# Kernel tuning notes

Measured on AMD Instinct MI355X. Metric: run time of the kernel, lower is better.

## Reference

```python
import jax, jax.numpy as jnp
import numpy as np

# Dimensions per init_kwargs
B, S, D = 2, 2048, 1024          # batch, seq, hidden_size
F = 4096                          # intermediate_size
E, K = 8, 2                       # moe_num_experts, moe_top_k
EPS = 1e-9


def setup_inputs() -> dict:
    key = jax.random.key(0)
    k1, k2, k3, k4 = jax.random.split(key, 4)
    x = jax.random.normal(k1, (B, S, D), dtype=jnp.float32)
    # gate: Linear(D, E, bias=False) -> stored as [D, E] for x @ w_gate
    w_gate = jax.random.normal(k2, (D, E), dtype=jnp.float32) * 0.02
    # per-expert gate_up_proj: Linear(D, 2F, bias=False), stacked over experts -> [E, D, 2F]
    w_gate_up = jax.random.normal(k3, (E, D, 2 * F), dtype=jnp.float32) * 0.02
    # per-expert down_proj: Linear(F, D, bias=False), stacked -> [E, F, D]
    w_down = jax.random.normal(k4, (E, F, D), dtype=jnp.float32) * 0.02
    return {"x": x, "w_gate": w_gate, "w_gate_up": w_gate_up, "w_down": w_down}


def reference(x, w_gate, w_gate_up, w_down):
    # Router
    gate_logits = x @ w_gate                       # [B,S,E]
    gate_probs = jax.nn.softmax(gate_logits, axis=-1)
    # top-k masking + renormalization (top_k < num_experts)
    topk_vals, topk_idx = jax.lax.top_k(gate_probs, K)           # [B,S,K]
    masked = jnp.sum(jax.nn.one_hot(topk_idx, E, dtype=gate_probs.dtype)
                     * topk_vals[..., None], axis=-2)            # [B,S,E]
    denom = jnp.maximum(jnp.sum(masked, axis=-1, keepdims=True), EPS)
    gate_probs = masked / denom

    # Dense per-expert SwiGLU FFN on all tokens (faithful to reference impl)
    gu = jnp.einsum('bsd,edh->ebsh', x, w_gate_up)               # [E,B,S,2F]
    g, u = jnp.split(gu, 2, axis=-1)                             # [E,B,S,F] each
    act = jax.nn.silu(g) * u                                     # [E,B,S,F]
    expert_out = jnp.einsum('ebsf,efd->ebsd', act, w_down)       # [E,B,S,D]

    # Gate-weighted combine
    return jnp.einsum('bse,ebsd->bsd', gate_probs, expert_out)   # [B,S,D]
```

## Files before the change

### kernel.cpp

```cpp
#include <hip/hip_runtime.h>
#include <stdint.h>

#define NTOK 4096
#define DMODEL 1024
#define FF 4096
#define NEXP 8

typedef __bf16 bf16x8 __attribute__((ext_vector_type(8)));
typedef float f32x4 __attribute__((ext_vector_type(4)));

__device__ __forceinline__ unsigned short f2bf(float f) {
  union { float f; unsigned u; } v; v.f = f;
  unsigned r = v.u + 0x7fffu + ((v.u >> 16) & 1u);
  return (unsigned short)(r >> 16);
}

__global__ __launch_bounds__(256) void k_convert_x(const float4* __restrict__ in,
                                                   ushort4* __restrict__ out, int n4) {
  int stride = gridDim.x * blockDim.x;
  for (int i = blockIdx.x * blockDim.x + threadIdx.x; i < n4; i += stride) {
    float4 v = in[i];
    out[i] = make_ushort4(f2bf(v.x), f2bf(v.y), f2bf(v.z), f2bf(v.w));
  }
}

__global__ __launch_bounds__(256) void k_transpose_bf16(const float* __restrict__ in,
                                                        unsigned short* __restrict__ out,
                                                        int R, int C) {
  __shared__ float tile[64][65];
  const size_t slab = (size_t)R * C;
  const float* ip = in + slab * blockIdx.z;
  unsigned short* op = out + slab * blockIdx.z;
  int c0 = blockIdx.x * 64, r0 = blockIdx.y * 64;
  int tx = threadIdx.x & 15, ty = threadIdx.x >> 4;
#pragma unroll
  for (int i = 0; i < 4; ++i) {
    int r = ty + 16 * i;
    float4 v = *(const float4*)(ip + (size_t)(r0 + r) * C + c0 + tx * 4);
    tile[r][tx * 4 + 0] = v.x;
    tile[r][tx * 4 + 1] = v.y;
    tile[r][tx * 4 + 2] = v.z;
    tile[r][tx * 4 + 3] = v.w;
  }
  __syncthreads();
#pragma unroll
  for (int i = 0; i < 4; ++i) {
    int q = ty + 16 * i;
    ushort4 o = make_ushort4(f2bf(tile[tx * 4 + 0][q]), f2bf(tile[tx * 4 + 1][q]),
                             f2bf(tile[tx * 4 + 2][q]), f2bf(tile[tx * 4 + 3][q]));
    *(ushort4*)(op + (size_t)(c0 + q) * R + r0 + tx * 4) = o;
  }
}

__global__ __launch_bounds__(256) void k_router(const float* __restrict__ x,
                                                const float* __restrict__ wg,
                                                int* __restrict__ cnt,
                                                int* __restrict__ elist,
                                                float* __restrict__ gw) {
  int wave = threadIdx.x >> 6, lane = threadIdx.x & 63;
  int t = blockIdx.x * 4 + wave;
  const float* xp = x + (size_t)t * DMODEL;
  float a[8] = {0, 0, 0, 0, 0, 0, 0, 0};
#pragma unroll
  for (int i = 0; i < DMODEL / 64; ++i) {
    int d = lane + 64 * i;
    float xv = xp[d];
    float4 w0 = *(const float4*)(wg + d * 8);
    float4 w1 = *(const float4*)(wg + d * 8 + 4);
    a[0] += xv * w0.x; a[1] += xv * w0.y; a[2] += xv * w0.z; a[3] += xv * w0.w;
    a[4] += xv * w1.x; a[5] += xv * w1.y; a[6] += xv * w1.z; a[7] += xv * w1.w;
  }
#pragma unroll
  for (int off = 32; off > 0; off >>= 1)
#pragma unroll
    for (int e = 0; e < 8; ++e) a[e] += __shfl_down(a[e], off, 64);
  if (lane == 0) {
    int e0 = 0;
    for (int e = 1; e < 8; ++e) if (a[e] > a[e0]) e0 = e;
    int e1 = (e0 == 0) ? 1 : 0;
    for (int e = 0; e < 8; ++e) if (e != e0 && a[e] > a[e1]) e1 = e;
    float p = __expf(a[e1] - a[e0]);
    float inv = 1.0f / (1.0f + p);
    int p0 = atomicAdd(&cnt[e0], 1);
    elist[e0 * NTOK + p0] = 2 * t;
    gw[2 * t] = inv;
    int p1 = atomicAdd(&cnt[e1], 1);
    elist[e1 * NTOK + p1] = 2 * t + 1;
    gw[2 * t + 1] = p * inv;
  }
}

__global__ __launch_bounds__(512, 2) void k_gemm1(const unsigned short* __restrict__ xb,
                                                  const unsigned short* __restrict__ wgu,
                                                  const int* __restrict__ cnt,
                                                  const int* __restrict__ elist,
                                                  unsigned short* __restrict__ act)
{
  __shared__ __align__(16) unsigned short sA[2][256 * 64];
  __shared__ __align__(16) unsigned short sB[2][256 * 64];

  const int e = blockIdx.z;
  const int n_e = cnt[e];
  const int m0 = blockIdx.y * 256;
  if (m0 >= n_e) return;
  const int c0 = blockIdx.x * 128;
  const int tid = threadIdx.x;
  const int w = tid >> 6, lane = tid & 63;
  const int wr = w >> 2, wc = w & 3;
  const int* el = elist + e * NTOK;
  const int csub = ((lane & 7) ^ (lane >> 3)) * 8;
  const int srow = w * 8 + (lane >> 3);

  int tokrow[4];
  size_t baddr[4];
  const unsigned short* wb = wgu + (size_t)e * (2 * FF) * DMODEL;
#pragma unroll
  for (int i = 0; i < 4; ++i) {
    int r = i * 64 + srow;
    int idx = m0 + r;
    tokrow[i] = el[idx < n_e ? idx : 0] >> 1;
    int strip = r >> 6, off = r & 63;
    int wrow = (off < 32) ? (c0 + strip * 32 + off) : (FF + c0 + strip * 32 + off - 32);
    baddr[i] = (size_t)wrow * DMODEL;
  }

  f32x4 acc[8][4];
  f32x4 zero = {0.f, 0.f, 0.f, 0.f};
#pragma unroll
  for (int m = 0; m < 8; ++m)
#pragma unroll
    for (int n = 0; n < 4; ++n) acc[m][n] = zero;

  auto stage = [&](int buf, int k0) {
#pragma unroll
    for (int i = 0; i < 4; ++i) {
      const unsigned short* g = xb + (size_t)tokrow[i] * DMODEL + k0 + csub;
      __builtin_amdgcn_global_load_lds((const __attribute__((address_space(1))) void*)g,
                                       (__attribute__((address_space(3))) void*)(&sA[buf][(i * 64 + w * 8) * 64]),
                                       16, 0, 0);
    }
#pragma unroll
    for (int i = 0; i < 4; ++i) {
      const unsigned short* g = wb + baddr[i] + k0 + csub;
      __builtin_amdgcn_global_load_lds((const __attribute__((address_space(1))) void*)g,
                                       (__attribute__((address_space(3))) void*)(&sB[buf][(i * 64 + w * 8) * 64]),
                                       16, 0, 0);
    }
  };

  auto compute = [&](int buf) {
#pragma unroll
    for (int kk = 0; kk < 2; ++kk) {
      const int xk = ((kk * 4 + (lane >> 4)) ^ (lane & 7)) * 8;
      bf16x8 af[8], bf[4];
#pragma unroll
      for (int m = 0; m < 8; ++m)
        af[m] = *(const bf16x8*)(&sA[buf][(wr * 128 + m * 16 + (lane & 15)) * 64 + xk]);
#pragma unroll
      for (int n = 0; n < 4; ++n)
        bf[n] = *(const bf16x8*)(&sB[buf][(wc * 64 + n * 16 + (lane & 15)) * 64 + xk]);
#pragma unroll
      for (int m = 0; m < 8; ++m)
#pragma unroll
        for (int n = 0; n < 4; ++n)
          acc[m][n] = __builtin_amdgcn_mfma_f32_16x16x32_bf16(af[m], bf[n], acc[m][n], 0, 0, 0);
    }
  };

  stage(0, 0);
  __syncthreads();
  int cur = 0;
  for (int t = 0; t < DMODEL / 64; ++t) {
    if (t + 1 < DMODEL / 64) stage(cur ^ 1, (t + 1) * 64);
    compute(cur);
    __syncthreads();
    cur ^= 1;
  }

#pragma unroll
  for (int m = 0; m < 8; ++m) {
#pragma unroll
    for (int r = 0; r < 4; ++r) {
      int idx = m0 + wr * 128 + m * 16 + (lane >> 4) * 4 + r;
      if (idx < n_e) {
        int p = el[idx];
        unsigned short* ap = act + (size_t)p * FF + c0 + wc * 32;
#pragma unroll
        for (int n = 0; n < 2; ++n) {
          float g = acc[m][n][r];
          float u = acc[m][n + 2][r];
          float s = g / (1.0f + __expf(-g));
          ap[n * 16 + (lane & 15)] = f2bf(s * u);
        }
      }
    }
  }
}

__global__ __launch_bounds__(512, 2) void k_gemm2(const unsigned short* __restrict__ actb,
                                                  const unsigned short* __restrict__ wd,
                                                  const int* __restrict__ cnt,
                                                  const int* __restrict__ elist,
                                                  const float* __restrict__ gw,
                                                  float* __restrict__ out_slot)
{
  __shared__ __align__(16) unsigned short sA[2][256 * 64];
  __shared__ __align__(16) unsigned short sB[2][128 * 64];

  const int e = blockIdx.z;
  const int n_e = cnt[e];
  const int m0 = blockIdx.y * 256;
  if (m0 >= n_e) return;
  const int n0 = blockIdx.x * 128;
  const int tid = threadIdx.x;
  const int w = tid >> 6, lane = tid & 63;
  const int wr = w >> 2, wc = w & 3;
  const int* el = elist + e * NTOK;
  const int csub = ((lane & 7) ^ (lane >> 3)) * 8;
  const int srow = w * 8 + (lane >> 3);

  int prow[4];
  size_t baddr[2];
  const unsigned short* wb = wd + (size_t)e * DMODEL * FF;
#pragma unroll
  for (int i = 0; i < 4; ++i) {
    int idx = m0 + i * 64 + srow;
    prow[i] = el[idx < n_e ? idx : 0];
  }
#pragma unroll
  for (int i = 0; i < 2; ++i)
    baddr[i] = (size_t)(n0 + i * 64 + srow) * FF;

  f32x4 acc[8][2];
  f32x4 zero = {0.f, 0.f, 0.f, 0.f};
#pragma unroll
  for (int m = 0; m < 8; ++m)
#pragma unroll
    for (int n = 0; n < 2; ++n) acc[m][n] = zero;

  auto stage = [&](int buf, int k0) {
#pragma unroll
    for (int i = 0; i < 4; ++i) {
      const unsigned short* g = actb + (size_t)prow[i] * FF + k0 + csub;
      __builtin_amdgcn_global_load_lds((const __attribute__((address_space(1))) void*)g,
                                       (__attribute__((address_space(3))) void*)(&sA[buf][(i * 64 + w * 8) * 64]),
                                       16, 0, 0);
    }
#pragma unroll
    for (int i = 0; i < 2; ++i) {
      const unsigned short* g = wb + baddr[i] + k0 + csub;
      __builtin_amdgcn_global_load_lds((const __attribute__((address_space(1))) void*)g,
                                       (__attribute__((address_space(3))) void*)(&sB[buf][(i * 64 + w * 8) * 64]),
                                       16, 0, 0);
    }
  };

  auto compute = [&](int buf) {
#pragma unroll
    for (int kk = 0; kk < 2; ++kk) {
      const int xk = ((kk * 4 + (lane >> 4)) ^ (lane & 7)) * 8;
      bf16x8 af[8], bf[2];
#pragma unroll
      for (int m = 0; m < 8; ++m)
        af[m] = *(const bf16x8*)(&sA[buf][(wr * 128 + m * 16 + (lane & 15)) * 64 + xk]);
#pragma unroll
      for (int n = 0; n < 2; ++n)
        bf[n] = *(const bf16x8*)(&sB[buf][(wc * 32 + n * 16 + (lane & 15)) * 64 + xk]);
#pragma unroll
      for (int m = 0; m < 8; ++m)
#pragma unroll
        for (int n = 0; n < 2; ++n)
          acc[m][n] = __builtin_amdgcn_mfma_f32_16x16x32_bf16(af[m], bf[n], acc[m][n], 0, 0, 0);
    }
  };

  stage(0, 0);
  __syncthreads();
  int cur = 0;
  for (int t = 0; t < FF / 64; ++t) {
    if (t + 1 < FF / 64) stage(cur ^ 1, (t + 1) * 64);
    compute(cur);
    __syncthreads();
    cur ^= 1;
  }

#pragma unroll
  for (int m = 0; m < 8; ++m) {
#pragma unroll
    for (int r = 0; r < 4; ++r) {
      int idx = m0 + wr * 128 + m * 16 + (lane >> 4) * 4 + r;
      if (idx < n_e) {
        int p = el[idx];
        float wgt = gw[p];
        float* op = out_slot + (size_t)p * DMODEL + n0 + wc * 32;
#pragma unroll
        for (int n = 0; n < 2; ++n)
          op[n * 16 + (lane & 15)] = acc[m][n][r] * wgt;
      }
    }
  }
}

__global__ __launch_bounds__(256) void k_combine(const float4* __restrict__ slot,
                                                 float4* __restrict__ out, int n4) {
  int stride = gridDim.x * blockDim.x;
  for (int i = blockIdx.x * blockDim.x + threadIdx.x; i < n4; i += stride) {
    int t = i >> 8;
    int j = i & 255;
    float4 a = slot[(size_t)(2 * t) * 256 + j];
    float4 b = slot[(size_t)(2 * t + 1) * 256 + j];
    float4 o;
    o.x = a.x + b.x; o.y = a.y + b.y; o.z = a.z + b.z; o.w = a.w + b.w;
    out[i] = o;
  }
}

extern "C" void kernel_launch(void* const* d_in, const int* in_sizes, int n_in,
                              void* d_out, int out_size, void* d_ws, size_t ws_size,
                              hipStream_t stream) {
  const float* x   = (const float*)d_in[0];
  const float* wg  = (const float*)d_in[1];
  const float* wgu = (const float*)d_in[2];
  const float* wd  = (const float*)d_in[3];
  float* out = (float*)d_out;

  char* ws = (char*)d_ws;
  size_t off = 0;
  auto alloc = [&](size_t bytes) -> char* {
    char* p = ws + off;
    off += (bytes + 255) & ~(size_t)255;
    return p;
  };
  unsigned short* wgu_t = (unsigned short*)alloc((size_t)NEXP * 2 * FF * DMODEL * 2);
  unsigned short* wd_t  = (unsigned short*)alloc((size_t)NEXP * DMODEL * FF * 2);
  unsigned short* actb  = (unsigned short*)alloc((size_t)2 * NTOK * FF * 2);
  float* out_slot       = (float*)alloc((size_t)2 * NTOK * DMODEL * 4);
  unsigned short* xb    = (unsigned short*)alloc((size_t)NTOK * DMODEL * 2);
  int* elist            = (int*)alloc((size_t)NEXP * NTOK * 4);
  float* gw             = (float*)alloc((size_t)2 * NTOK * 4);
  int* cnt              = (int*)alloc(256);
  if (off > ws_size) return;

  hipMemsetAsync(cnt, 0, 256, stream);
  k_convert_x<<<1024, 256, 0, stream>>>((const float4*)x, (ushort4*)xb, NTOK * DMODEL / 4);
  k_transpose_bf16<<<dim3(2 * FF / 64, DMODEL / 64, NEXP), 256, 0, stream>>>(wgu, wgu_t, DMODEL, 2 * FF);
  k_transpose_bf16<<<dim3(DMODEL / 64, FF / 64, NEXP), 256, 0, stream>>>(wd, wd_t, FF, DMODEL);
  k_router<<<NTOK / 4, 256, 0, stream>>>(x, wg, cnt, elist, gw);
  k_gemm1<<<dim3(FF / 128, NTOK / 256, NEXP), 512, 0, stream>>>(xb, wgu_t, cnt, elist, actb);
  k_gemm2<<<dim3(DMODEL / 128, NTOK / 256, NEXP), 512, 0, stream>>>(actb, wd_t, cnt, elist, gw, out_slot);
  k_combine<<<2048, 256, 0, stream>>>((const float4*)out_slot, (float4*)out, NTOK * DMODEL / 4);
}
```

Before: 640.5 us.

## Interleave staged global-to-LDS loads with quarter-tile MFMA phases in both expert GEMMs

Both expert GEMM kernels now split each K-step into four sub-phases over half-M by half-N quadrants. Each phase first reads its fragments from LDS, then issues a slice of the next tile's global-to-LDS loads, and then runs the MFMAs at raised wave priority, with explicit vmcnt waits and barriers in place of one syncthreads per tile. The B-tile rows are remapped so that each load slice fills exactly the quadrant consumed later. The aim is to spread memory traffic across the compute and keep the MFMA pipe busier, at the cost of more barriers per K-step and fragile hand-placed vmcnt counts.

After: 679.2 us. +6.0%, slower.

```diff
diff --git a/kernel.cpp b/kernel.cpp
--- a/kernel.cpp
+++ b/kernel.cpp
@@ -109,19 +109,25 @@
   const int wr = w >> 2, wc = w & 3;
   const int* el = elist + e * NTOK;
   const int csub = ((lane & 7) ^ (lane >> 3)) * 8;
-  const int srow = w * 8 + (lane >> 3);
 
   int tokrow[4];
-  size_t baddr[4];
   const unsigned short* wb = wgu + (size_t)e * (2 * FF) * DMODEL;
 #pragma unroll
   for (int i = 0; i < 4; ++i) {
-    int r = i * 64 + srow;
-    int idx = m0 + r;
+    int idx = m0 + i * 64 + w * 8 + (lane >> 3);
     tokrow[i] = el[idx < n_e ? idx : 0] >> 1;
+  }
+  size_t baddrB[4];
+  int ldsBrow[4];
+#pragma unroll
+  for (int j = 0; j < 4; ++j) {
+    const int bb4[4] = {0, 128, 32, 160};
+    int rbase = bb4[j] + w * 8 + ((w >> 2) * 32);
+    int r = rbase + (lane >> 3);
     int strip = r >> 6, off = r & 63;
     int wrow = (off < 32) ? (c0 + strip * 32 + off) : (FF + c0 + strip * 32 + off - 32);
-    baddr[i] = (size_t)wrow * DMODEL;
+    baddrB[j] = (size_t)wrow * DMODEL;
+    ldsBrow[j] = rbase;
   }
 
   f32x4 acc[8][4];
@@ -131,50 +137,65 @@
 #pragma unroll
     for (int n = 0; n < 4; ++n) acc[m][n] = zero;
 
-  auto stage = [&](int buf, int k0) {
-#pragma unroll
-    for (int i = 0; i < 4; ++i) {
-      const unsigned short* g = xb + (size_t)tokrow[i] * DMODEL + k0 + csub;
-      __builtin_amdgcn_global_load_lds((const __attribute__((address_space(1))) void*)g,
-                                       (__attribute__((address_space(3))) void*)(&sA[buf][(i * 64 + w * 8) * 64]),
-                                       16, 0, 0);
+  auto stageA = [&](int buf, int k0, int i) {
+    const unsigned short* g = xb + (size_t)tokrow[i] * DMODEL + k0 + csub;
+    __builtin_amdgcn_global_load_lds((const __attribute__((address_space(1))) void*)g,
+                                     (__attribute__((address_space(3))) void*)(&sA[buf][(i * 64 + w * 8) * 64]),
+                                     16, 0, 0);
+  };
+  auto stageB = [&](int buf, int k0, int j) {
+    const unsigned short* g = wb + baddrB[j] + k0 + csub;
+    __builtin_amdgcn_global_load_lds((const __attribute__((address_space(1))) void*)g,
+                                     (__attribute__((address_space(3))) void*)(&sB[buf][ldsBrow[j] * 64]),
+                                     16, 0, 0);
+  };
+  auto stagePart = [&](int buf, int k0, int part) {
+    if (part == 0)      { stageA(buf, k0, 0); stageA(buf, k0, 2); }
+    else if (part == 1) { stageB(buf, k0, 0); stageB(buf, k0, 1); }
+    else if (part == 2) { stageA(buf, k0, 1); stageA(buf, k0, 3); }
+    else                { stageB(buf, k0, 2); stageB(buf, k0, 3); }
+  };
+
+  const int NT = DMODEL / 64;
+#pragma unroll
+  for (int part = 0; part < 4; ++part) stagePart(0, 0, part);
+  asm volatile("s_waitcnt vmcnt(4)" ::: "memory");
+  __builtin_amdgcn_s_barrier();
+
+  for (int t = 0; t < NT; ++t) {
+    const int buf = t & 1;
+    const int nk0 = (t + 1) * 64;
+    const bool pre = (t + 1 < NT);
+#pragma unroll
+    for (int p = 0; p < 4; ++p) {
+      const int mh = p & 1, nh = p >> 1;
+      bf16x8 af[4][2], bfr[2][2];
+#pragma unroll
+      for (int kk = 0; kk < 2; ++kk) {
+        const int xk = ((kk * 4 + (lane >> 4)) ^ (lane & 7)) * 8;
+#pragma unroll
+        for (int m = 0; m < 4; ++m)
+          af[m][kk] = *(const bf16x8*)(&sA[buf][(wr * 128 + mh * 64 + m * 16 + (lane & 15)) * 64 + xk]);
+#pragma unroll
+        for (int n = 0; n < 2; ++n)
+          bfr[n][kk] = *(const bf16x8*)(&sB[buf][(wc * 64 + nh * 32 + n * 16 + (lane & 15)) * 64 + xk]);
+      }
+      if (pre) stagePart(buf ^ 1, nk0, p);
+      __builtin_amdgcn_s_barrier();
+      __builtin_amdgcn_s_setprio(1);
+#pragma unroll
+      for (int kk = 0; kk < 2; ++kk)
+#pragma unroll
+        for (int m = 0; m < 4; ++m)
+#pragma unroll
+          for (int n = 0; n < 2; ++n)
+            acc[mh * 4 + m][nh * 2 + n] =
+                __builtin_amdgcn_mfma_f32_16x16x32_bf16(af[m][kk], bfr[n][kk],
+                                                        acc[mh * 4 + m][nh * 2 + n], 0, 0, 0);
+      __builtin_amdgcn_s_setprio(0);
+      asm volatile("s_waitcnt vmcnt(4)" ::: "memory");
+      __builtin_amdgcn_s_barrier();
     }
-#pragma unroll
-    for (int i = 0; i < 4; ++i) {
-      const unsigned short* g = wb + baddr[i] + k0 + csub;
-      __builtin_amdgcn_global_load_lds((const __attribute__((address_space(1))) void*)g,
-                                       (__attribute__((address_space(3))) void*)(&sB[buf][(i * 64 + w * 8) * 64]),
-                                       16, 0, 0);
-    }
-  };
-
-  auto compute = [&](int buf) {
-#pragma unroll
-    for (int kk = 0; kk < 2; ++kk) {
-      const int xk = ((kk * 4 + (lane >> 4)) ^ (lane & 7)) * 8;
-      bf16x8 af[8], bf[4];
-#pragma unroll
-      for (int m = 0; m < 8; ++m)
-        af[m] = *(const bf16x8*)(&sA[buf][(wr * 128 + m * 16 + (lane & 15)) * 64 + xk]);
-#pragma unroll
-      for (int n = 0; n < 4; ++n)
-        bf[n] = *(const bf16x8*)(&sB[buf][(wc * 64 + n * 16 + (lane & 15)) * 64 + xk]);
-#pragma unroll
-      for (int m = 0; m < 8; ++m)
-#pragma unroll
-        for (int n = 0; n < 4; ++n)
-          acc[m][n] = __builtin_amdgcn_mfma_f32_16x16x32_bf16(af[m], bf[n], acc[m][n], 0, 0, 0);
-    }
-  };
-
-  stage(0, 0);
-  __syncthreads();
-  int cur = 0;
-  for (int t = 0; t < DMODEL / 64; ++t) {
-    if (t + 1 < DMODEL / 64) stage(cur ^ 1, (t + 1) * 64);
-    compute(cur);
-    __syncthreads();
-    cur ^= 1;
   }
 
 #pragma unroll
@@ -217,19 +238,22 @@
   const int wr = w >> 2, wc = w & 3;
   const int* el = elist + e * NTOK;
   const int csub = ((lane & 7) ^ (lane >> 3)) * 8;
-  const int srow = w * 8 + (lane >> 3);
 
   int prow[4];
-  size_t baddr[2];
   const unsigned short* wb = wd + (size_t)e * DMODEL * FF;
 #pragma unroll
   for (int i = 0; i < 4; ++i) {
-    int idx = m0 + i * 64 + srow;
+    int idx = m0 + i * 64 + w * 8 + (lane >> 3);
     prow[i] = el[idx < n_e ? idx : 0];
   }
-#pragma unroll
-  for (int i = 0; i < 2; ++i)
-    baddr[i] = (size_t)(n0 + i * 64 + srow) * FF;
+  size_t baddrB[2];
+  int ldsBrow[2];
+#pragma unroll
+  for (int j = 0; j < 2; ++j) {
+    int rbase = (w >> 1) * 32 + (w & 1) * 8 + j * 16;
+    baddrB[j] = (size_t)(n0 + rbase + (lane >> 3)) * FF;
+    ldsBrow[j] = rbase;
+  }
 
   f32x4 acc[8][2];
   f32x4 zero = {0.f, 0.f, 0.f, 0.f};
@@ -238,50 +262,61 @@
 #pragma unroll
     for (int n = 0; n < 2; ++n) acc[m][n] = zero;
 
-  auto stage = [&](int buf, int k0) {
-#pragma unroll
-    for (int i = 0; i < 4; ++i) {
-      const unsigned short* g = actb + (size_t)prow[i] * FF + k0 + csub;
-      __builtin_amdgcn_global_load_lds((const __attribute__((address_space(1))) void*)g,
-                                       (__attribute__((address_space(3))) void*)(&sA[buf][(i * 64 + w * 8) * 64]),
-                                       16, 0, 0);
+  auto stageA = [&](int buf, int k0, int i) {
+    const unsigned short* g = actb + (size_t)prow[i] * FF + k0 + csub;
+    __builtin_amdgcn_global_load_lds((const __attribute__((address_space(1))) void*)g,
+                                     (__attribute__((address_space(3))) void*)(&sA[buf][(i * 64 + w * 8) * 64]),
+                                     16, 0, 0);
+  };
+  auto stageB = [&](int buf, int k0, int j) {
+    const unsigned short* g = wb + baddrB[j] + k0 + csub;
+    __builtin_amdgcn_global_load_lds((const __attribute__((address_space(1))) void*)g,
+                                     (__attribute__((address_space(3))) void*)(&sB[buf][ldsBrow[j] * 64]),
+                                     16, 0, 0);
+  };
+  auto stagePart = [&](int buf, int k0, int part) {
+    if (part == 0)      { stageA(buf, k0, 0); stageA(buf, k0, 2); }
+    else if (part == 1) { stageB(buf, k0, 0); }
+    else if (part == 2) { stageA(buf, k0, 1); stageA(buf, k0, 3); }
+    else                { stageB(buf, k0, 1); }
+  };
+
+  const int NT = FF / 64;
+#pragma unroll
+  for (int part = 0; part < 4; ++part) stagePart(0, 0, part);
+  asm volatile("s_waitcnt vmcnt(3)" ::: "memory");
+  __builtin_amdgcn_s_barrier();
+
+  for (int t = 0; t < NT; ++t) {
+    const int buf = t & 1;
+    const int nk0 = (t + 1) * 64;
+    const bool pre = (t + 1 < NT);
+#pragma unroll
+    for (int p = 0; p < 4; ++p) {
+      const int mh = p & 1, nh = p >> 1;
+      bf16x8 af[4][2], bfr[2];
+#pragma unroll
+      for (int kk = 0; kk < 2; ++kk) {
+        const int xk = ((kk * 4 + (lane >> 4)) ^ (lane & 7)) * 8;
+#pragma unroll
+        for (int m = 0; m < 4; ++m)
+          af[m][kk] = *(const bf16x8*)(&sA[buf][(wr * 128 + mh * 64 + m * 16 + (lane & 15)) * 64 + xk]);
+        bfr[kk] = *(const bf16x8*)(&sB[buf][(wc * 32 + nh * 16 + (lane & 15)) * 64 + xk]);
+      }
+      if (pre) stagePart(buf ^ 1, nk0, p);
+      __builtin_amdgcn_s_barrier();
+      __builtin_amdgcn_s_setprio(1);
+#pragma unroll
+      for (int kk = 0; kk < 2; ++kk)
+#pragma unroll
+        for (int m = 0; m < 4; ++m)
+          acc[mh * 4 + m][nh] =
+              __builtin_amdgcn_mfma_f32_16x16x32_bf16(af[m][kk], bfr[kk],
+                                                      acc[mh * 4 + m][nh], 0, 0, 0);
+      __builtin_amdgcn_s_setprio(0);
+      asm volatile("s_waitcnt vmcnt(3)" ::: "memory");
+      __builtin_amdgcn_s_barrier();
     }
-#pragma unroll
-    for (int i = 0; i < 2; ++i) {
-      const unsigned short* g = wb + baddr[i] + k0 + csub;
-      __builtin_amdgcn_global_load_lds((const __attribute__((address_space(1))) void*)g,
-                                       (__attribute__((address_space(3))) void*)(&sB[buf][(i * 64 + w * 8) * 64]),
-                                       16, 0, 0);
-    }
-  };
-
-  auto compute = [&](int buf) {
-#pragma unroll
-    for (int kk = 0; kk < 2; ++kk) {
-      const int xk = ((kk * 4 + (lane >> 4)) ^ (lane & 7)) * 8;
-      bf16x8 af[8], bf[2];
-#pragma unroll
-      for (int m = 0; m < 8; ++m)
-        af[m] = *(const bf16x8*)(&sA[buf][(wr * 128 + m * 16 + (lane & 15)) * 64 + xk]);
-#pragma unroll
-      for (int n = 0; n < 2; ++n)
-        bf[n] = *(const bf16x8*)(&sB[buf][(wc * 32 + n * 16 + (lane & 15)) * 64 + xk]);
-#pragma unroll
-      for (int m = 0; m < 8; ++m)
-#pragma unroll
-        for (int n = 0; n < 2; ++n)
-          acc[m][n] = __builtin_amdgcn_mfma_f32_16x16x32_bf16(af[m], bf[n], acc[m][n], 0, 0, 0);
-    }
-  };
-
-  stage(0, 0);
-  __syncthreads();
-  int cur = 0;
-  for (int t = 0; t < FF / 64; ++t) {
-    if (t + 1 < FF / 64) stage(cur ^ 1, (t + 1) * 64);
-    compute(cur);
-    __syncthreads();
-    cur ^= 1;
   }
 
 #pragma unroll
```

## Shrink gemm2 tiles to 128x128 with 256 threads and single-buffered LDS

Applied to the files above, without the earlier changes.

The down-projection GEMM moves from 256x128 tiles with 512 threads and double-buffered LDS to 128x128 tiles with 256 threads and one LDS buffer, synchronising before and after each k-step. The aim is more blocks per expert, better load balance across the uneven per-expert token counts, and lower LDS use for higher occupancy. In exchange, global loads no longer overlap compute within a block, and each block reuses less data per tile, so reliance on other resident blocks to hide latency grows.

Result: faster. 619.3 us (-3.3%).

```diff
diff --git a/kernel.cpp b/kernel.cpp
--- a/kernel.cpp
+++ b/kernel.cpp
@@ -197,104 +197,91 @@
   }
 }
 
-__global__ __launch_bounds__(512, 2) void k_gemm2(const unsigned short* __restrict__ actb,
-                                                  const unsigned short* __restrict__ wd,
-                                                  const int* __restrict__ cnt,
-                                                  const int* __restrict__ elist,
-                                                  const float* __restrict__ gw,
-                                                  float* __restrict__ out_slot)
+__global__ __launch_bounds__(256) void k_gemm2(const unsigned short* __restrict__ actb,
+                                               const unsigned short* __restrict__ wd,
+                                               const int* __restrict__ cnt,
+                                               const int* __restrict__ elist,
+                                               const float* __restrict__ gw,
+                                               float* __restrict__ out_slot)
 {
-  __shared__ __align__(16) unsigned short sA[2][256 * 64];
-  __shared__ __align__(16) unsigned short sB[2][128 * 64];
+  __shared__ __align__(16) unsigned short sA[128 * 64];
+  __shared__ __align__(16) unsigned short sB[128 * 64];
 
   const int e = blockIdx.z;
   const int n_e = cnt[e];
-  const int m0 = blockIdx.y * 256;
+  const int m0 = blockIdx.y * 128;
   if (m0 >= n_e) return;
   const int n0 = blockIdx.x * 128;
   const int tid = threadIdx.x;
   const int w = tid >> 6, lane = tid & 63;
-  const int wr = w >> 2, wc = w & 3;
+  const int wr = w >> 1, wc = w & 1;
   const int* el = elist + e * NTOK;
   const int csub = ((lane & 7) ^ (lane >> 3)) * 8;
-  const int srow = w * 8 + (lane >> 3);
 
   int prow[4];
-  size_t baddr[2];
+  size_t baddr[4];
   const unsigned short* wb = wd + (size_t)e * DMODEL * FF;
 #pragma unroll
   for (int i = 0; i < 4; ++i) {
-    int idx = m0 + i * 64 + srow;
+    int r = i * 32 + w * 8 + (lane >> 3);
+    int idx = m0 + r;
     prow[i] = el[idx < n_e ? idx : 0];
-  }
-#pragma unroll
-  for (int i = 0; i < 2; ++i)
-    baddr[i] = (size_t)(n0 + i * 64 + srow) * FF;
-
-  f32x4 acc[8][2];
+    baddr[i] = (size_t)(n0 + r) * FF;
+  }
+
+  f32x4 acc[4][4];
   f32x4 zero = {0.f, 0.f, 0.f, 0.f};
 #pragma unroll
-  for (int m = 0; m < 8; ++m)
-#pragma unroll
-    for (int n = 0; n < 2; ++n) acc[m][n] = zero;
-
-  auto stage = [&](int buf, int k0) {
+  for (int m = 0; m < 4; ++m)
+#pragma unroll
+    for (int n = 0; n < 4; ++n) acc[m][n] = zero;
+
+  for (int k0 = 0; k0 < FF; k0 += 64) {
 #pragma unroll
     for (int i = 0; i < 4; ++i) {
       const unsigned short* g = actb + (size_t)prow[i] * FF + k0 + csub;
       __builtin_amdgcn_global_load_lds((const __attribute__((address_space(1))) void*)g,
-                                       (__attribute__((address_space(3))) void*)(&sA[buf][(i * 64 + w * 8) * 64]),
+                                       (__attribute__((address_space(3))) void*)(&sA[(i * 32 + w * 8) * 64]),
                                        16, 0, 0);
     }
 #pragma unroll
-    for (int i = 0; i < 2; ++i) {
+    for (int i = 0; i < 4; ++i) {
       const unsigned short* g = wb + baddr[i] + k0 + csub;
       __builtin_amdgcn_global_load_lds((const __attribute__((address_space(1))) void*)g,
-                                       (__attribute__((address_space(3))) void*)(&sB[buf][(i * 64 + w * 8) * 64]),
+                                       (__attribute__((address_space(3))) void*)(&sB[(i * 32 + w * 8) * 64]),
                                        16, 0, 0);
     }
-  };
-
-  auto compute = [&](int buf) {
+    __syncthreads();
 #pragma unroll
     for (int kk = 0; kk < 2; ++kk) {
       const int xk = ((kk * 4 + (lane >> 4)) ^ (lane & 7)) * 8;
-      bf16x8 af[8], bf[2];
-#pragma unroll
-      for (int m = 0; m < 8; ++m)
-        af[m] = *(const bf16x8*)(&sA[buf][(wr * 128 + m * 16 + (lane & 15)) * 64 + xk]);
-#pragma unroll
-      for (int n = 0; n < 2; ++n)
-        bf[n] = *(const bf16x8*)(&sB[buf][(wc * 32 + n * 16 + (lane & 15)) * 64 + xk]);
-#pragma unroll
-      for (int m = 0; m < 8; ++m)
-#pragma unroll
-        for (int n = 0; n < 2; ++n)
+      bf16x8 af[4], bf[4];
+#pragma unroll
+      for (int m = 0; m < 4; ++m)
+        af[m] = *(const bf16x8*)(&sA[(wr * 64 + m * 16 + (lane & 15)) * 64 + xk]);
+#pragma unroll
+      for (int n = 0; n < 4; ++n)
+        bf[n] = *(const bf16x8*)(&sB[(wc * 64 + n * 16 + (lane & 15)) * 64 + xk]);
+#pragma unroll
+      for (int m = 0; m < 4; ++m)
+#pragma unroll
+        for (int n = 0; n < 4; ++n)
           acc[m][n] = __builtin_amdgcn_mfma_f32_16x16x32_bf16(af[m], bf[n], acc[m][n], 0, 0, 0);
     }
-  };
-
-  stage(0, 0);
-  __syncthreads();
-  int cur = 0;
-  for (int t = 0; t < FF / 64; ++t) {
-    if (t + 1 < FF / 64) stage(cur ^ 1, (t + 1) * 64);
-    compute(cur);
     __syncthreads();
-    cur ^= 1;
-  }
-
-#pragma unroll
-  for (int m = 0; m < 8; ++m) {
+  }
+
+#pragma unroll
+  for (int m = 0; m < 4; ++m) {
 #pragma unroll
     for (int r = 0; r < 4; ++r) {
-      int idx = m0 + wr * 128 + m * 16 + (lane >> 4) * 4 + r;
+      int idx = m0 + wr * 64 + m * 16 + (lane >> 4) * 4 + r;
       if (idx < n_e) {
         int p = el[idx];
         float wgt = gw[p];
-        float* op = out_slot + (size_t)p * DMODEL + n0 + wc * 32;
-#pragma unroll
-        for (int n = 0; n < 2; ++n)
+        float* op = out_slot + (size_t)p * DMODEL + n0 + wc * 64;
+#pragma unroll
+        for (int n = 0; n < 4; ++n)
           op[n * 16 + (lane & 15)] = acc[m][n][r] * wgt;
       }
     }
@@ -347,6 +334,6 @@
   k_transpose_bf16<<<dim3(DMODEL / 64, FF / 64, NEXP), 256, 0, stream>>>(wd, wd_t, FF, DMODEL);
   k_router<<<NTOK / 4, 256, 0, stream>>>(x, wg, cnt, elist, gw);
   k_gemm1<<<dim3(FF / 128, NTOK / 256, NEXP), 512, 0, stream>>>(xb, wgu_t, cnt, elist, actb);
-  k_gemm2<<<dim3(DMODEL / 128, NTOK / 256, NEXP), 512, 0, stream>>>(actb, wd_t, cnt, elist, gw, out_slot);
+  k_gemm2<<<dim3(DMODEL / 128, NTOK / 128, NEXP), 256, 0, stream>>>(actb, wd_t, cnt, elist, gw, out_slot);
   k_combine<<<2048, 256, 0, stream>>>((const float4*)out_slot, (float4*)out, NTOK * DMODEL / 4);
 }
```
